# Kernel tuning notes

Hardware: AMD Instinct MI355X
Metric: run time of the kernel (lower is better)

The kernel has to match this reference:

```python
import jax, jax.numpy as jnp
import numpy as np
from jax import lax

PR = [0.0, -39.68, -3.0, 69.12, 39.68, 1.0]  # POINT_CLOUD_RANGE
SIZE = (1024, 1024)  # (W, H)
B = 4
NBF = 64
BN_EPS = 1e-5


def setup_inputs() -> dict:
    key = jax.random.key(0)
    ks = jax.random.split(key, 16)
    N = 800_000
    bidx = jax.random.randint(ks[0], (N,), 0, B).astype(jnp.float32)
    x = jax.random.uniform(ks[1], (N,), minval=PR[0], maxval=PR[3])
    y = jax.random.uniform(ks[2], (N,), minval=PR[1], maxval=PR[4])
    z = jax.random.uniform(ks[3], (N,), minval=PR[2], maxval=PR[5])
    inten = jax.random.uniform(ks[4], (N,))
    points = jnp.stack([bidx, x, y, z, inten], axis=1)
    params = {}
    chans = [(4, 8), (8, 16), (16, 32), (32, NBF)]
    for li, (ci, co) in enumerate(chans, start=1):
        kk = jax.random.split(ks[5 + li], 6)
        params[f"w{li}"] = jax.random.normal(kk[0], (co, ci, 3, 3)) * (1.0 / np.sqrt(ci * 9))
        params[f"b{li}"] = jax.random.normal(kk[1], (co,)) * 0.01
        params[f"g{li}"] = jax.random.uniform(kk[2], (co,), minval=0.5, maxval=1.5)
        params[f"be{li}"] = jax.random.normal(kk[3], (co,)) * 0.01
        params[f"m{li}"] = jax.random.normal(kk[4], (co,)) * 0.01
        params[f"v{li}"] = jax.random.uniform(kk[5], (co,), minval=0.5, maxval=1.5)
    return {"points": points, "batch_size": 4, **params}


def _points_to_bev(points, batch_size):
    # Faithful to points_to_bevs_all (returned channels: count/50, zmin, zmax, intensity;
    # bev_average_z is computed but never returned in the original, so it is omitted).
    W, H = SIZE
    xs = W / (PR[3] - PR[0])
    ys = H / (PR[4] - PR[1])
    # PR[0] == 0 branch of the original
    xp = (points[:, 1] * xs).astype(jnp.int32)
    yp = ((points[:, 2] + (PR[4] - PR[1]) / 2) * ys).astype(jnp.int32)
    b = points[:, 0].astype(jnp.int32)
    mask = (xp >= 0) & (xp < W) & (yp >= 0) & (yp < H)
    lin = jnp.where(mask, (b * H + yp) * W + xp, 0)  # flat [B*H*W] index
    z = points[:, 3]
    inten = points[:, 4]
    n = batch_size * H * W
    neg = jnp.float32(-jnp.inf)
    pos = jnp.float32(jnp.inf)
    cnt = jnp.zeros((n,), jnp.float32).at[lin].add(mask.astype(jnp.float32))
    zmax = jnp.full((n,), -10.0, jnp.float32).at[lin].max(jnp.where(mask, z, neg))
    zmin = jnp.full((n,), 10.0, jnp.float32).at[lin].min(jnp.where(mask, z, pos))
    iv = jnp.zeros((n,), jnp.float32).at[lin].max(jnp.where(mask, inten, neg))
    bev = jnp.where(cnt == 0, 1.0, cnt) / 50.0
    stacked = jnp.stack([bev, zmin, zmax, iv], axis=0).reshape(4, batch_size, H, W)
    return jnp.transpose(stacked, (1, 0, 2, 3))  # [B,4,H,W]


def _cbr(x, w, b, g, be, m, v):
    # Conv(3x3, stride 1, pad 1) + BatchNorm (inference) + ReLU
    y = lax.conv_general_dilated(x, w, (1, 1), 'SAME',
                                 dimension_numbers=('NCHW', 'OIHW', 'NCHW'))
    y = y + b[:, None, None]
    scale = (g / jnp.sqrt(v + BN_EPS))[:, None, None]
    y = (y - m[:, None, None]) * scale + be[:, None, None]
    return jax.nn.relu(y)


def _pool(x):
    return lax.reduce_window(x, -jnp.inf, lax.max, (1, 1, 2, 2), (1, 1, 2, 2), 'VALID')


def reference(points, batch_size,
              w1, b1, g1, be1, m1, v1,
              w2, b2, g2, be2, m2, v2,
              w3, b3, g3, be3, m3, v3,
              w4, b4, g4, be4, m4, v4):
    bev = _points_to_bev(points, batch_size)  # [B,4,1024,1024]
    x = _pool(_cbr(bev, w1, b1, g1, be1, m1, v1))  # [B,8,512,512]
    x = _pool(_cbr(x, w2, b2, g2, be2, m2, v2))    # [B,16,256,256]
    x = _pool(_cbr(x, w3, b3, g3, be3, m3, v3))    # [B,32,128,128]
    return _cbr(x, w4, b4, g4, be4, m4, v4)        # [B,64,128,128] spatial_features
```

## Files before the change

kernel.cpp:

```cpp
#include <hip/hip_runtime.h>
#include <cstdint>
#include <cstddef>

#define HH 1024
#define WW 1024
#define NB 4

typedef _Float16 half8 __attribute__((ext_vector_type(8)));
typedef _Float16 half4 __attribute__((ext_vector_type(4)));
typedef float f32x4 __attribute__((ext_vector_type(4)));
typedef unsigned long long ull;

__global__ __launch_bounds__(256)
void clear_cells(float4* __restrict__ p, int n4) {
  int stride = gridDim.x * blockDim.x;
  float4 z; z.x = 0.f; z.y = 0.f; z.z = 0.f; z.w = 0.f;
  for (int i = blockIdx.x * blockDim.x + threadIdx.x; i < n4; i += stride)
    p[i] = z;
}

__device__ __forceinline__ unsigned merge_cell(unsigned a, unsigned zq,
                                               unsigned zn, unsigned iq) {
  unsigned cnt = a & 0xFFu;
  unsigned civ = (a >> 8) & 0xFFu;
  unsigned czn = (a >> 16) & 0xFFu;
  unsigned czx = a >> 24;
  cnt = (cnt < 255u) ? cnt + 1u : cnt;
  civ = civ > iq ? civ : iq;
  czn = czn > zn ? czn : zn;
  czx = czx > zq ? czx : zq;
  return cnt | (civ << 8) | (czn << 16) | (czx << 24);
}

__global__ __launch_bounds__(256)
void scatter_points_packed(const float* __restrict__ pts, int n,
                           unsigned* __restrict__ cell) {
  const float xs   = (float)(1024.0 / 69.12);
  const float ys   = (float)(1024.0 / (39.68 + 39.68));
  const float yoff = 39.68f;
  int i = blockIdx.x * blockDim.x + threadIdx.x;
  if (i >= n) return;
  float b  = pts[(size_t)i * 5 + 0];
  float x  = pts[(size_t)i * 5 + 1];
  float y  = pts[(size_t)i * 5 + 2];
  float z  = pts[(size_t)i * 5 + 3];
  float it = pts[(size_t)i * 5 + 4];
  int xp = (int)(x * xs);
  int yp = (int)((y + yoff) * ys);
  if (xp < 0 || xp >= WW || yp < 0 || yp >= HH) return;
  int lin = ((int)b * HH + yp) * WW + xp;

  float zc = fminf(fmaxf(z, -3.f), 1.f);
  unsigned zq = (unsigned)(int)((zc + 3.f) * (255.f / 4.f) + 0.5f);
  if (zq > 255u) zq = 255u;
  float ic = fminf(fmaxf(it, 0.f), 1.f);
  unsigned iq = (unsigned)(int)(ic * 255.f + 0.5f);
  if (iq > 255u) iq = 255u;
  unsigned zn = 255u - zq;

  unsigned g = atomicCAS(&cell[lin], 0u, merge_cell(0u, zq, zn, iq));
  while (g != 0u) {
    unsigned r = atomicCAS(&cell[lin], g, merge_cell(g, zq, zn, iq));
    if (r == g) break;
    g = r;
  }
}

template<int CI, int CIp, int COT, int COp, int HWI, int PXT, int KS,
         bool POOL, int INMODE, bool OUTCL>
__global__ __launch_bounds__(512)
void conv_mfma(const void* __restrict__ in, void* __restrict__ outv,
               const float* __restrict__ wgt, const float* __restrict__ bias,
               const float* __restrict__ gam, const float* __restrict__ bet,
               const float* __restrict__ mean, const float* __restrict__ var) {
  constexpr int PYT  = 32;
  constexpr int NTHR = 512;
  constexpr int NT   = COp / 16;
  constexpr int XH   = PXT / 16;
  constexpr int NCOL = PXT + 2;
  constexpr int NCELL = (PYT + 2) * NCOL;
  constexpr int WROW = KS * 32 + 8;
  constexpr int INE  = NCELL * CIp;
  constexpr int L2C  = (CIp == 8) ? 3 : ((CIp == 16) ? 4 : 5);
  constexpr int KTOT = 9 * CIp;
  constexpr int COR  = (COT < COp) ? COT : COp;
  constexpr int PXH  = PXT / 2;
  constexpr int OCS  = 136;
  static_assert(CIp % 8 == 0 && COp % 16 == 0, "");
  static_assert(INMODE != 0 || (CI == 4 && CIp == 8 && KS == 2), "");
  static_assert(!OUTCL || (POOL && COT % 8 == 0), "");
  static_assert(!POOL || 16 * PXH * COp * 2 <= INE * 2, "out overlay fits");
  static_assert(POOL || COp * OCS * 4 <= INE * 2, "out overlay fits");

  __shared__ __align__(16) char s_raw[INE * 2 + COp * WROW * 2 + COp * 8];
  _Float16* s_in = (_Float16*)s_raw;
  _Float16* s_w  = (_Float16*)(s_raw + INE * 2);
  float* s_scale = (float*)(s_raw + INE * 2 + (size_t)COp * WROW * 2);
  float* s_shift = s_scale + COp;

  const int cobase = blockIdx.y * COp;
  const int b = blockIdx.z;
  constexpr int NPX = HWI / PXT;
  const int pyi = blockIdx.x / NPX;
  const int pxi = blockIdx.x - pyi * NPX;
  const int y0 = pyi * PYT, x0 = pxi * PXT;

  half8 zv;
  #pragma unroll
  for (int q = 0; q < 8; ++q) zv[q] = (_Float16)0.f;

  if constexpr (INMODE == 0) {
    const unsigned* pin = (const unsigned*)in;
    for (int t = threadIdx.x; t < NCELL; t += NTHR) {
      int col = t % NCOL;
      int row = t / NCOL;
      int gy = y0 - 1 + row, gx = x0 - 1 + col;
      half4 v;
      v[0] = (_Float16)0.f; v[1] = (_Float16)0.f;
      v[2] = (_Float16)0.f; v[3] = (_Float16)0.f;
      if (gy >= 0 && gy < HH && gx >= 0 && gx < WW) {
        unsigned pv = pin[((size_t)b * HH + gy) * WW + gx];
        unsigned cnt = pv & 0xFFu;
        unsigned ivq = (pv >> 8) & 0xFFu;
        unsigned znq = (pv >> 16) & 0xFFu;
        unsigned zxq = pv >> 24;
        float c0, c1, c2, c3;
        if (cnt == 0) { c0 = 0.02f; c1 = 10.f; c2 = -10.f; c3 = 0.f; }
        else {
          c0 = (float)cnt * 0.02f;
          c1 = (float)(255u - znq) * (4.0f / 255.0f) - 3.0f;
          c2 = (float)zxq * (4.0f / 255.0f) - 3.0f;
          c3 = (float)ivq * (1.0f / 255.0f);
        }
        v[0] = (_Float16)c0; v[1] = (_Float16)c1;
        v[2] = (_Float16)c2; v[3] = (_Float16)c3;
      }
      *(half4*)&s_in[(size_t)t * 8] = v;
      if (col > 0)
        *(half4*)&s_in[(size_t)(t - 1) * 8 + 4] = v;
      if (col == NCOL - 1) {
        half4 z4;
        z4[0] = (_Float16)0.f; z4[1] = (_Float16)0.f;
        z4[2] = (_Float16)0.f; z4[3] = (_Float16)0.f;
        *(half4*)&s_in[(size_t)t * 8 + 4] = z4;
      }
    }
  } else {
    const _Float16* fin = (const _Float16*)in;
    for (int t = threadIdx.x; t < NCELL; t += NTHR) {
      int col = t % NCOL;
      int row = t / NCOL;
      int gy = y0 - 1 + row, gx = x0 - 1 + col;
      bool okc = (gy >= 0 && gy < HWI && gx >= 0 && gx < HWI);
      int swz = (CIp == 8) ? 0 : ((CIp == 16) ? ((col >> 2) & 1) : ((col >> 1) & 3));
      #pragma unroll
      for (int c8 = 0; c8 < CIp / 8; ++c8) {
        half8 v = zv;
        if (okc)
          v = *(const half8*)((const _Float16*)fin +
                (((size_t)b * HWI + gy) * HWI + gx) * CI + c8 * 8);
        *(half8*)&s_in[(size_t)t * CIp + ((c8 ^ swz) << 3)] = v;
      }
    }
  }
  if constexpr (INMODE == 0) {
    for (int t = threadIdx.x; t < COp * KS * 32; t += NTHR) {
      int k   = t % (KS * 32);
      int col = t / (KS * 32);
      int cog = cobase + col;
      int p = k >> 3, j = k & 7;
      float v = 0.f;
      if (p < 6 && cog < COT) {
        int tA = p + ((p + 1) >> 1);
        int ci = j & 3;
        if (j < 4) v = wgt[((size_t)cog * CI + ci) * 9 + tA];
        else if ((p & 1) == 0) v = wgt[((size_t)cog * CI + ci) * 9 + tA + 1];
      }
      s_w[col * WROW + k] = (_Float16)v;
    }
  } else {
    for (int t = threadIdx.x; t < COp * KS * 32; t += NTHR) {
      int k   = t % (KS * 32);
      int col = t / (KS * 32);
      int cog = cobase + col;
      float v = 0.f;
      if (k < KTOT && cog < COT) {
        int tap = k / CIp, ci = k % CIp;
        if (ci < CI) v = wgt[((size_t)cog * CI + ci) * 9 + tap];
      }
      s_w[col * WROW + k] = (_Float16)v;
    }
  }
  if (threadIdx.x < COp) {
    int col = threadIdx.x;
    int cog = cobase + col;
    float sc = 0.f, sh = 0.f;
    if (cog < COT) {
      sc = gam[cog] / sqrtf(var[cog] + 1e-5f);
      sh = (bias[cog] - mean[cog]) * sc + bet[cog];
    }
    s_scale[col] = sc; s_shift[col] = sh;
  }
  __syncthreads();

  const int lane = threadIdx.x & 63;
  const int w    = threadIdx.x >> 6;
  const int m    = lane & 15;
  const int hi   = lane >> 4;

  f32x4 acc[4][XH][NT];
  #pragma unroll
  for (int r = 0; r < 4; ++r)
    #pragma unroll
    for (int h = 0; h < XH; ++h)
      #pragma unroll
      for (int n = 0; n < NT; ++n) acc[r][h][n] = 0.f;

  const int y0w = w * 4;
  #pragma unroll
  for (int ks = 0; ks < KS; ++ks) {
    int aoff;
    if constexpr (INMODE == 0) {
      int p = ks * 4 + hi;
      if (p > 5) p = 5;
      int dy  = p >> 1;
      int dxA = (p & 1) << 1;
      aoff = ((y0w + dy) * NCOL + m + dxA) * 8;
    } else {
      int kc  = ks * 32 + (hi << 3);
      int tap = kc >> L2C;
      if (tap > 8) tap = 8;
      int ci  = kc & (CIp - 1);
      int dy  = (tap * 11) >> 5;
      int dx  = tap - 3 * dy;
      int colA  = m + dx;
      int chunk = ci >> 3;
      int swz = (CIp == 8) ? 0 : ((CIp == 16) ? ((colA >> 2) & 1) : ((colA >> 1) & 3));
      aoff = ((y0w + dy) * NCOL + colA) * CIp + ((chunk ^ swz) << 3);
    }
    const int boff = m * WROW + ks * 32 + (hi << 3);
    half8 bfr[NT];
    #pragma unroll
    for (int n = 0; n < NT; ++n)
      bfr[n] = *(const half8*)&s_w[boff + n * 16 * WROW];
    #pragma unroll
    for (int r = 0; r < 4; ++r) {
      half8 afr[XH];
      #pragma unroll
      for (int h = 0; h < XH; ++h)
        afr[h] = *(const half8*)&s_in[aoff + r * NCOL * CIp + h * 16 * CIp];
      #pragma unroll
      for (int h = 0; h < XH; ++h)
        #pragma unroll
        for (int n = 0; n < NT; ++n)
          acc[r][h][n] = __builtin_amdgcn_mfma_f32_16x16x32_f16(
              afr[h], bfr[n], acc[r][h][n], 0, 0, 0);
    }
  }

  __syncthreads();

  if constexpr (POOL) {
    _Float16* s_o = (_Float16*)s_raw;
    #pragma unroll
    for (int n = 0; n < NT; ++n) {
      int col = n * 16 + m;
      float sc = s_scale[col], sh = s_shift[col];
      #pragma unroll
      for (int rp = 0; rp < 2; ++rp) {
        #pragma unroll
        for (int h = 0; h < XH; ++h) {
          f32x4 p0 = acc[rp * 2][h][n];
          f32x4 p1 = acc[rp * 2 + 1][h][n];
          float v0 = fmaxf(fmaxf(p0[0], p0[1]), fmaxf(p1[0], p1[1]));
          float v1 = fmaxf(fmaxf(p0[2], p0[3]), fmaxf(p1[2], p1[3]));
          v0 = fmaxf(v0 * sc + sh, 0.f);
          v1 = fmaxf(v1 * sc + sh, 0.f);
          int yp = w * 2 + rp;
          int xp = h * 8 + hi * 2;
          s_o[(yp * PXH + xp) * COp + col]     = (_Float16)v0;
          s_o[(yp * PXH + xp + 1) * COp + col] = (_Float16)v1;
        }
      }
    }
    __syncthreads();
    constexpr int HWO = HWI / 2;
    constexpr int NCHG = (COR + 7) / 8;
    _Float16* og = (_Float16*)outv;
    for (int t = threadIdx.x; t < 16 * PXH * NCHG; t += NTHR) {
      int c8  = t % NCHG;
      int rem = t / NCHG;
      int xp  = rem % PXH;
      int yp  = rem / PXH;
      half8 v = *(const half8*)&s_o[(yp * PXH + xp) * COp + c8 * 8];
      *(half8*)&og[(((size_t)b * HWO + (y0 / 2 + yp)) * HWO + (x0 / 2 + xp)) * COT
                   + cobase + c8 * 8] = v;
    }
  } else {
    float* s_out = (float*)s_raw;
    float* og = (float*)outv;
    #pragma unroll
    for (int r = 0; r < 4; ++r) {
      if (r) __syncthreads();
      #pragma unroll
      for (int n = 0; n < NT; ++n) {
        int col = n * 16 + m;
        float sc = s_scale[col], sh = s_shift[col];
        f32x4 p = acc[r][0][n];
        #pragma unroll
        for (int q = 0; q < 4; ++q) {
          float v = fmaxf(p[q] * sc + sh, 0.f);
          s_out[col * OCS + w * 16 + hi * 4 + q] = v;
        }
      }
      __syncthreads();
      for (int t = threadIdx.x; t < COR * 8 * 16; t += NTHR) {
        int xp = t & 15, ws3 = (t >> 4) & 7, col = t >> 7;
        og[(((size_t)b * COT + cobase + col) * HWI + (y0 + ws3 * 4 + r)) * HWI + (x0 + xp)]
          = s_out[col * OCS + ws3 * 16 + xp];
      }
    }
  }
}

extern "C" void kernel_launch(void* const* d_in, const int* in_sizes, int n_in,
                              void* d_out, int out_size, void* d_ws, size_t ws_size,
                              hipStream_t stream) {
  const float* pts = (const float*)d_in[0];
  const int npts = in_sizes[0] / 5;

  const float* w1  = (const float*)d_in[2];
  const float* b1  = (const float*)d_in[3];
  const float* g1  = (const float*)d_in[4];
  const float* be1 = (const float*)d_in[5];
  const float* m1  = (const float*)d_in[6];
  const float* v1  = (const float*)d_in[7];
  const float* w2  = (const float*)d_in[8];
  const float* b2  = (const float*)d_in[9];
  const float* g2  = (const float*)d_in[10];
  const float* be2 = (const float*)d_in[11];
  const float* m2  = (const float*)d_in[12];
  const float* v2  = (const float*)d_in[13];
  const float* w3  = (const float*)d_in[14];
  const float* b3  = (const float*)d_in[15];
  const float* g3  = (const float*)d_in[16];
  const float* be3 = (const float*)d_in[17];
  const float* m3  = (const float*)d_in[18];
  const float* v3  = (const float*)d_in[19];
  const float* w4  = (const float*)d_in[20];
  const float* b4  = (const float*)d_in[21];
  const float* g4  = (const float*)d_in[22];
  const float* be4 = (const float*)d_in[23];
  const float* m4  = (const float*)d_in[24];
  const float* v4  = (const float*)d_in[25];

  char* ws = (char*)d_ws;
  unsigned* packed = (unsigned*)ws;
  void* l1 = (void*)(ws + 33554432);
  void* l2 = (void*)(ws + 50331648);
  void* l3 = (void*)(ws + 58720256);
  void* outp = d_out;

  clear_cells<<<2048, 256, 0, stream>>>((float4*)packed, (int)((size_t)NB * HH * WW * 4 / 16));
  scatter_points_packed<<<(npts + 255) / 256, 256, 0, stream>>>(pts, npts, packed);

  conv_mfma<4,  8,  8,  16, 1024, 64, 2, true,  0, true ><<<dim3(512, 1, 4), 512, 0, stream>>>(packed, l1, w1, b1, g1, be1, m1, v1);
  conv_mfma<8,  8,  16, 16, 512,  64, 3, true,  1, true ><<<dim3(128, 1, 4), 512, 0, stream>>>(l1,  l2, w2, b2, g2, be2, m2, v2);
  conv_mfma<16, 16, 32, 16, 256,  32, 5, true,  1, true ><<<dim3(64,  2, 4), 512, 0, stream>>>(l2,  l3, w3, b3, g3, be3, m3, v3);
  conv_mfma<32, 32, 64, 16, 128,  16, 9, false, 1, false><<<dim3(32,  4, 4), 512, 0, stream>>>(l3, outp, w4, b4, g4, be4, m4, v4);
}
```

Before: 95.38 us.

## Compute even/odd output columns via split weights in first conv layer

```diff
diff --git a/kernel.cpp b/kernel.cpp
--- a/kernel.cpp
+++ b/kernel.cpp
@@ -76,18 +76,19 @@
   constexpr int PYT  = 32;
   constexpr int NTHR = 512;
   constexpr int NT   = COp / 16;
-  constexpr int XH   = PXT / 16;
+  constexpr int XH   = (INMODE == 0) ? (PXT / 32) : (PXT / 16);
   constexpr int NCOL = PXT + 2;
+  constexpr int NSLOT = (INMODE == 0) ? ((NCOL + 1) / 2) : NCOL;
   constexpr int NCELL = (PYT + 2) * NCOL;
   constexpr int WROW = KS * 32 + 8;
-  constexpr int INE  = NCELL * CIp;
+  constexpr int INE  = (PYT + 2) * NSLOT * CIp;
   constexpr int L2C  = (CIp == 8) ? 3 : ((CIp == 16) ? 4 : 5);
   constexpr int KTOT = 9 * CIp;
   constexpr int COR  = (COT < COp) ? COT : COp;
   constexpr int PXH  = PXT / 2;
   constexpr int OCS  = 136;
   static_assert(CIp % 8 == 0 && COp % 16 == 0, "");
-  static_assert(INMODE != 0 || (CI == 4 && CIp == 8 && KS == 2), "");
+  static_assert(INMODE != 0 || (CI == 4 && CIp == 8 && KS == 2 && COT == 8 && COp == 16), "");
   static_assert(!OUTCL || (POOL && COT % 8 == 0), "");
   static_assert(!POOL || 16 * PXH * COp * 2 <= INE * 2, "out overlay fits");
   static_assert(POOL || COp * OCS * 4 <= INE * 2, "out overlay fits");
@@ -135,15 +136,7 @@
         v[0] = (_Float16)c0; v[1] = (_Float16)c1;
         v[2] = (_Float16)c2; v[3] = (_Float16)c3;
       }
-      *(half4*)&s_in[(size_t)t * 8] = v;
-      if (col > 0)
-        *(half4*)&s_in[(size_t)(t - 1) * 8 + 4] = v;
-      if (col == NCOL - 1) {
-        half4 z4;
-        z4[0] = (_Float16)0.f; z4[1] = (_Float16)0.f;
-        z4[2] = (_Float16)0.f; z4[3] = (_Float16)0.f;
-        *(half4*)&s_in[(size_t)t * 8 + 4] = z4;
-      }
+      *(half4*)&s_in[((size_t)row * NSLOT + (col >> 1)) * 8 + (col & 1) * 4] = v;
     }
   } else {
     const _Float16* fin = (const _Float16*)in;
@@ -167,14 +160,23 @@
     for (int t = threadIdx.x; t < COp * KS * 32; t += NTHR) {
       int k   = t % (KS * 32);
       int col = t / (KS * 32);
-      int cog = cobase + col;
       int p = k >> 3, j = k & 7;
+      int ci = j & 3;
       float v = 0.f;
-      if (p < 6 && cog < COT) {
-        int tA = p + ((p + 1) >> 1);
-        int ci = j & 3;
-        if (j < 4) v = wgt[((size_t)cog * CI + ci) * 9 + tA];
-        else if ((p & 1) == 0) v = wgt[((size_t)cog * CI + ci) * 9 + tA + 1];
+      if (p < 6) {
+        int dy = p >> 1;
+        if (col < 8) {
+          int tA = p + ((p + 1) >> 1);
+          if (j < 4) v = wgt[((size_t)col * CI + ci) * 9 + tA];
+          else if ((p & 1) == 0) v = wgt[((size_t)col * CI + ci) * 9 + tA + 1];
+        } else {
+          int co = col - 8;
+          if ((p & 1) == 0) {
+            if (j >= 4) v = wgt[((size_t)co * CI + ci) * 9 + dy * 3 + 0];
+          } else {
+            v = wgt[((size_t)co * CI + ci) * 9 + dy * 3 + ((j < 4) ? 1 : 2)];
+          }
+        }
       }
       s_w[col * WROW + k] = (_Float16)v;
     }
@@ -193,7 +195,7 @@
   }
   if (threadIdx.x < COp) {
     int col = threadIdx.x;
-    int cog = cobase + col;
+    int cog = (INMODE == 0) ? (col & 7) : (cobase + col);
     float sc = 0.f, sh = 0.f;
     if (cog < COT) {
       sc = gam[cog] / sqrtf(var[cog] + 1e-5f);
@@ -223,9 +225,8 @@
     if constexpr (INMODE == 0) {
       int p = ks * 4 + hi;
       if (p > 5) p = 5;
-      int dy  = p >> 1;
-      int dxA = (p & 1) << 1;
-      aoff = ((y0w + dy) * NCOL + m + dxA) * 8;
+      int dy = p >> 1;
+      aoff = ((y0w + dy) * NSLOT + m + (p & 1)) * 8;
     } else {
       int kc  = ks * 32 + (hi << 3);
       int tap = kc >> L2C;
@@ -236,7 +237,7 @@
       int colA  = m + dx;
       int chunk = ci >> 3;
       int swz = (CIp == 8) ? 0 : ((CIp == 16) ? ((colA >> 2) & 1) : ((colA >> 1) & 3));
-      aoff = ((y0w + dy) * NCOL + colA) * CIp + ((chunk ^ swz) << 3);
+      aoff = ((y0w + dy) * NSLOT + colA) * CIp + ((chunk ^ swz) << 3);
     }
     const int boff = m * WROW + ks * 32 + (hi << 3);
     half8 bfr[NT];
@@ -248,19 +249,52 @@
       half8 afr[XH];
       #pragma unroll
       for (int h = 0; h < XH; ++h)
-        afr[h] = *(const half8*)&s_in[aoff + r * NCOL * CIp + h * 16 * CIp];
+        afr[h] = *(const half8*)&s_in[aoff + r * NSLOT * CIp + h * 16 * CIp];
+      __builtin_amdgcn_s_setprio(1);
       #pragma unroll
       for (int h = 0; h < XH; ++h)
         #pragma unroll
         for (int n = 0; n < NT; ++n)
           acc[r][h][n] = __builtin_amdgcn_mfma_f32_16x16x32_f16(
               afr[h], bfr[n], acc[r][h][n], 0, 0, 0);
+      __builtin_amdgcn_s_setprio(0);
     }
   }
 
   __syncthreads();
 
-  if constexpr (POOL) {
+  if constexpr (POOL && INMODE == 0) {
+    _Float16* s_o = (_Float16*)s_raw;
+    float sc = s_scale[m & 7], sh = s_shift[m & 7];
+    #pragma unroll
+    for (int rp = 0; rp < 2; ++rp) {
+      #pragma unroll
+      for (int h = 0; h < XH; ++h) {
+        f32x4 p0 = acc[rp * 2][h][0];
+        f32x4 p1 = acc[rp * 2 + 1][h][0];
+        #pragma unroll
+        for (int q = 0; q < 4; ++q) {
+          float ym = fmaxf(p0[q], p1[q]);
+          float part = __shfl_xor(ym, 8);
+          if (m < 8) {
+            float v = fmaxf(fmaxf(ym, part) * sc + sh, 0.f);
+            int yp = w * 2 + rp;
+            int xp = h * 16 + hi * 4 + q;
+            s_o[(yp * PXH + xp) * COp + m] = (_Float16)v;
+          }
+        }
+      }
+    }
+    __syncthreads();
+    constexpr int HWO = HWI / 2;
+    _Float16* og = (_Float16*)outv;
+    for (int t = threadIdx.x; t < 16 * PXH; t += NTHR) {
+      int xp = t % PXH;
+      int yp = t / PXH;
+      half8 v = *(const half8*)&s_o[(yp * PXH + xp) * COp];
+      *(half8*)&og[(((size_t)b * HWO + (y0 / 2 + yp)) * HWO + (x0 / 2 + xp)) * COT] = v;
+    }
+  } else if constexpr (POOL) {
     _Float16* s_o = (_Float16*)s_raw;
     #pragma unroll
     for (int n = 0; n < NT; ++n) {
```

Result: no change. 93.87 us (-1.6%).
